# Kernel tuning notes

Measured on AMD Instinct MI355X. Metric: run time of the kernel, lower is better.

Reference implementation:

```python
import jax, jax.numpy as jnp
import numpy as np

IN_CH, C_M, C_N = 512, 512, 128
B, H, W = 16, 56, 56


def setup_inputs() -> dict:
    key = jax.random.key(0)
    ks = jax.random.split(key, 7)
    s = 1.0 / np.sqrt(IN_CH)
    return {
        "x": jax.random.normal(ks[0], (B, IN_CH, H, W), dtype=jnp.float32),
        "wA": jax.random.uniform(ks[1], (C_M, IN_CH), jnp.float32, -s, s),
        "bA": jax.random.uniform(ks[2], (C_M,), jnp.float32, -s, s),
        "wB": jax.random.uniform(ks[3], (C_N, IN_CH), jnp.float32, -s, s),
        "bB": jax.random.uniform(ks[4], (C_N,), jnp.float32, -s, s),
        "wV": jax.random.uniform(ks[5], (C_N, IN_CH), jnp.float32, -s, s),
        "bV": jax.random.uniform(ks[6], (C_N,), jnp.float32, -s, s),
        "K": 1,
    }


def reference(x, wA, bA, wB, bB, wV, bV, K):
    b, c, h, w = x.shape
    c_m, c_n = wA.shape[0], wB.shape[0]
    batch = b // K
    hw = h * w
    N = K * hw
    # 1x1 convs == channel-wise matmuls
    A = jnp.einsum('bchw,mc->bmhw', x, wA) + bA[None, :, None, None]
    Bf = jnp.einsum('bchw,nc->bnhw', x, wB) + bB[None, :, None, None]
    Vf = jnp.einsum('bchw,nc->bnhw', x, wV) + bV[None, :, None, None]
    # (batch, c_m, K*h*w)
    tmpA = A.reshape(batch, K, c_m, hw).transpose(0, 2, 1, 3).reshape(batch, c_m, N)
    # softmax over the spatial dim N (torch Softmax() on 2D -> dim=1)
    tmpB = Bf.reshape(batch, K, c_n, hw).transpose(0, 2, 1, 3).reshape(batch, c_n, N)
    attB = jax.nn.softmax(tmpB, axis=-1).transpose(0, 2, 1)  # (batch, N, c_n)
    # softmax over channel dim c_n
    tmpV = Vf.reshape(batch, K, c_n, hw).transpose(0, 1, 3, 2).reshape(batch, N, c_n)
    attV = jax.nn.softmax(tmpV, axis=-1).transpose(0, 2, 1)  # (batch, c_n, N)
    G = jnp.matmul(tmpA, attB)   # (batch, c_m, c_n) global descriptors
    Z = jnp.matmul(G, attV)      # (batch, c_m, N) distribute
    Z = Z.reshape(batch, c_m, K, hw).transpose(0, 2, 1, 3).reshape(b, c_m, h, w)
    return Z
```

## Files before the change

kernel.cpp:

```cpp
#include <hip/hip_runtime.h>
#include <hip/hip_bf16.h>

#define BATCH 16
#define CIN   512
#define HW    3136
#define CM    512
#define CN    128

typedef short short8 __attribute__((ext_vector_type(8)));
typedef float f32x4  __attribute__((ext_vector_type(4)));

#define MFMA(a,b,c) __builtin_amdgcn_mfma_f32_16x16x32_bf16((a),(b),(c),0,0,0)

__device__ __forceinline__ void cvt_store8(__bf16* dst, const float* src) {
  const f32x4 a = *(const f32x4*)src;
  const f32x4 b = *(const f32x4*)(src + 4);
  __attribute__((aligned(16))) __bf16 t[8];
  t[0] = (__bf16)a[0]; t[1] = (__bf16)a[1]; t[2] = (__bf16)a[2]; t[3] = (__bf16)a[3];
  t[4] = (__bf16)b[0]; t[5] = (__bf16)b[1]; t[6] = (__bf16)b[2]; t[7] = (__bf16)b[3];
  *(uint4*)dst = *(uint4*)t;
}

__device__ __forceinline__ void cvt_store8v(__bf16* dst, f32x4 a, f32x4 b) {
  __attribute__((aligned(16))) __bf16 t[8];
  t[0] = (__bf16)a[0]; t[1] = (__bf16)a[1]; t[2] = (__bf16)a[2]; t[3] = (__bf16)a[3];
  t[4] = (__bf16)b[0]; t[5] = (__bf16)b[1]; t[6] = (__bf16)b[2]; t[7] = (__bf16)b[3];
  *(uint4*)dst = *(uint4*)t;
}

__global__ __launch_bounds__(256) void prep_w_kernel(
    const float* __restrict__ wB, const float* __restrict__ wV,
    __bf16* __restrict__ Wimg)
{
  const int gid  = blockIdx.x * 256 + threadIdx.x;
  const int lane = gid & 63;
  const int kk   = (gid >> 6) & 1;
  const int mi   = (gid >> 7) & 3;
  const int w    = (gid >> 9) & 3;
  const int st   = (gid >> 11) & 7;
  const int row  = w*64 + mi*16 + (lane & 15);
  const int col  = st*64 + kk*32 + (lane >> 4)*8;
  const float* src = (row < 128) ? (wB + (size_t)row * CIN)
                                 : (wV + (size_t)(row - 128) * CIN);
  cvt_store8(Wimg + (size_t)gid * 8, src + col);
}

__global__ __launch_bounds__(256) void conv_bv_kernel(
    const float* __restrict__ x,
    const __bf16* __restrict__ Wimg,
    const float* __restrict__ bB, const float* __restrict__ bV,
    __bf16* __restrict__ BVB, __bf16* __restrict__ attVT,
    float* __restrict__ bsum)
{
  const int s0  = blockIdx.x * 64;
  const int b   = blockIdx.y;
  const int tid = threadIdx.x;
  const int lane = tid & 63, w = tid >> 6;
  const int l15  = lane & 15, q = lane >> 4;

  __shared__ __attribute__((aligned(16))) __bf16 Xt[2][64*72];
  __bf16* T = (__bf16*)Xt;
  __shared__ float Vm[2][64];
  __shared__ float Vs[2][64];

  f32x4 acc[4][4] = {};
  const float* xb = x + (size_t)b*CIN*HW + s0;
  const int colg = tid & 7;
  const int cl = 2*(tid >> 3);
  const int xoff = ((cl >> 3) ^ colg)*8 + (cl & 7);

  const char* wbase = (const char*)Wimg + (size_t)w*8192 + (size_t)lane*16;

  short8 wf[8];
#define WLOAD(ST) do { const char* wp_ = wbase + (ST)*32768; \
    wf[0]=*(const short8*)(wp_+0);    wf[1]=*(const short8*)(wp_+1024); \
    wf[2]=*(const short8*)(wp_+2048); wf[3]=*(const short8*)(wp_+3072); \
    wf[4]=*(const short8*)(wp_+4096); wf[5]=*(const short8*)(wp_+5120); \
    wf[6]=*(const short8*)(wp_+6144); wf[7]=*(const short8*)(wp_+7168); } while(0)

  f32x4 pf[2][4];
#define XLOAD(PB, K0) do { \
    const float* r0_ = xb + (size_t)((K0) + cl)*HW + colg*8; \
    const float* r1_ = r0_ + HW; \
    pf[PB][0] = *(const f32x4*)r0_; pf[PB][1] = *(const f32x4*)(r0_ + 4); \
    pf[PB][2] = *(const f32x4*)r1_; pf[PB][3] = *(const f32x4*)(r1_ + 4); } while(0)

#define XWRITE(BUF, PB) do { \
    _Pragma("unroll") \
    for (int j = 0; j < 8; ++j) { \
      int s_ = colg*8 + j; \
      union { __bf16 h[2]; unsigned int u; } pv_; \
      pv_.h[0] = (__bf16)pf[PB][j>>2][j&3]; \
      pv_.h[1] = (__bf16)pf[PB][2 + (j>>2)][j&3]; \
      *(unsigned int*)&Xt[BUF][s_*72 + xoff] = pv_.u; \
    } } while(0)

  XLOAD(0, 0);
  WLOAD(0);
  XLOAD(1, 64);
  XWRITE(0, 0);
  __syncthreads();

  #pragma unroll
  for (int st = 0; st < 8; ++st) {
    const int cur = st & 1;
    short8 xf0[4];
    #pragma unroll
    for (int si = 0; si < 4; ++si) {
      int s = si*16 + l15;
      int oct = q ^ (si*2 + (l15 >> 3));
      xf0[si] = *(short8*)&Xt[cur][s*72 + oct*8];
    }
    #pragma unroll
    for (int mi = 0; mi < 4; ++mi)
      #pragma unroll
      for (int si = 0; si < 4; ++si)
        acc[mi][si] = MFMA(wf[mi*2], xf0[si], acc[mi][si]);

    if (st < 7) XWRITE(cur ^ 1, (st + 1) & 1);
    if (st < 6) XLOAD(st & 1, (st + 2) * 64);

    short8 xf1[4];
    #pragma unroll
    for (int si = 0; si < 4; ++si) {
      int s = si*16 + l15;
      int oct = (4 + q) ^ (si*2 + (l15 >> 3));
      xf1[si] = *(short8*)&Xt[cur][s*72 + oct*8];
    }
    #pragma unroll
    for (int mi = 0; mi < 4; ++mi)
      #pragma unroll
      for (int si = 0; si < 4; ++si)
        acc[mi][si] = MFMA(wf[mi*2+1], xf1[si], acc[mi][si]);

    if (st < 7) WLOAD(st + 1);
    __syncthreads();
  }
#undef WLOAD
#undef XLOAD
#undef XWRITE

  float bias[4][4];
  #pragma unroll
  for (int mi = 0; mi < 4; ++mi)
    #pragma unroll
    for (int r = 0; r < 4; ++r) {
      int nch = w*64 + mi*16 + q*4 + r;
      bias[mi][r] = (nch < CN) ? bB[nch] : bV[nch - CN];
    }

  if (w < 2) {
    const size_t outb = (size_t)b * CN * HW;
    float psum[4][4] = {};
    #pragma unroll
    for (int mi = 0; mi < 4; ++mi)
      #pragma unroll
      for (int si = 0; si < 4; ++si) {
        int s = s0 + si*16 + l15;
        #pragma unroll
        for (int r = 0; r < 4; ++r) {
          int nch = w*64 + mi*16 + q*4 + r;
          __bf16 bv = (__bf16)(acc[mi][si][r] + bias[mi][r]);
          BVB[outb + (size_t)nch*HW + s] = bv;
          psum[mi][r] += __expf((float)bv);
        }
      }
    #pragma unroll
    for (int mi = 0; mi < 4; ++mi)
      #pragma unroll
      for (int r = 0; r < 4; ++r) {
        float v = psum[mi][r];
        v += __shfl_xor(v, 1); v += __shfl_xor(v, 2);
        v += __shfl_xor(v, 4); v += __shfl_xor(v, 8);
        if (l15 == 0) {
          int nch = w*64 + mi*16 + q*4 + r;
          atomicAdd(&bsum[b*CN + nch], v);
        }
      }
  } else {
    #pragma unroll
    for (int si = 0; si < 4; ++si) {
      float m = -1e30f;
      #pragma unroll
      for (int mi = 0; mi < 4; ++mi)
        #pragma unroll
        for (int r = 0; r < 4; ++r)
          m = fmaxf(m, acc[mi][si][r] + bias[mi][r]);
      m = fmaxf(m, __shfl_xor(m, 16));
      m = fmaxf(m, __shfl_xor(m, 32));
      if (q == 0) Vm[w-2][si*16 + l15] = m;
    }
  }
  __syncthreads();
  if (w >= 2) {
    #pragma unroll
    for (int si = 0; si < 4; ++si) {
      int idx = si*16 + l15;
      float ms = fmaxf(Vm[0][idx], Vm[1][idx]);
      float ssum = 0.f;
      #pragma unroll
      for (int mi = 0; mi < 4; ++mi)
        #pragma unroll
        for (int r = 0; r < 4; ++r) {
          float e = __expf(acc[mi][si][r] + bias[mi][r] - ms);
          acc[mi][si][r] = e;
          ssum += e;
        }
      ssum += __shfl_xor(ssum, 16);
      ssum += __shfl_xor(ssum, 32);
      if (q == 0) Vs[w-2][idx] = ssum;
    }
  }
  __syncthreads();
  if (w >= 2) {
    #pragma unroll
    for (int si = 0; si < 4; ++si) {
      int idx = si*16 + l15;
      float inv = 1.0f / (Vs[0][idx] + Vs[1][idx]);
      #pragma unroll
      for (int mi = 0; mi < 4; ++mi)
        #pragma unroll
        for (int r = 0; r < 4; ++r) {
          int j = (w-2)*64 + mi*16 + q*4 + r;
          T[idx*136 + j] = (__bf16)(acc[mi][si][r] * inv);
        }
    }
  }
  __syncthreads();
  __bf16* dst = attVT + ((size_t)b*HW + s0)*CN;
  #pragma unroll
  for (int k = 0; k < 4; ++k) {
    int chunk = tid + 256*k;
    int row = chunk >> 4, oct = chunk & 15;
    *(uint4*)&dst[(size_t)row*CN + oct*8] = *(uint4*)&T[row*136 + oct*8];
  }
}

__global__ __launch_bounds__(256) void h_gemm_kernel(
    const float* __restrict__ x, const __bf16* __restrict__ BVB,
    const float* __restrict__ bsum, float* __restrict__ H)
{
  const int c0 = blockIdx.x * 64, b = blockIdx.y, kc = blockIdx.z;
  const int tid = threadIdx.x, lane = tid & 63, w = tid >> 6;
  const int l15 = lane & 15, q = lane >> 4;

  __shared__ __attribute__((aligned(16))) __bf16 At[64*72];
  __shared__ __attribute__((aligned(16))) __bf16 Bt[128*72];
  f32x4 acc[4][2] = {};

  const float* xb = x + ((size_t)b*CIN + c0)*HW;
  const __bf16* ab = BVB + (size_t)b*CN*HW;
  const float* bsb = bsum + b*CN;
  const int colg = tid & 7, row0 = tid >> 3;

  float irow[4];
  #pragma unroll
  for (int p = 0; p < 4; ++p) irow[p] = 1.0f / bsb[row0 + 32*p];

  f32x4 px[2][2];
  uint4 pB[4];
#define HLOAD(K0) do { \
    _Pragma("unroll") \
    for (int p = 0; p < 2; ++p) { \
      const float* s_ = xb + (size_t)(row0 + 32*p)*HW + (K0) + colg*8; \
      px[p][0] = *(const f32x4*)s_; px[p][1] = *(const f32x4*)(s_ + 4); \
    } \
    _Pragma("unroll") \
    for (int p = 0; p < 4; ++p) \
      pB[p] = *(const uint4*)(ab + (size_t)(row0 + 32*p)*HW + (K0) + colg*8); \
  } while(0)

  const int kbase = kc * 448;
  HLOAD(kbase);

  for (int ki = 0; ki < 7; ++ki) {
    #pragma unroll
    for (int p = 0; p < 2; ++p)
      cvt_store8v(&At[(row0 + 32*p)*72 + colg*8], px[p][0], px[p][1]);
    #pragma unroll
    for (int p = 0; p < 4; ++p) {
      const __bf16* v = (const __bf16*)&pB[p];
      __attribute__((aligned(16))) __bf16 t[8];
      #pragma unroll
      for (int j = 0; j < 8; ++j)
        t[j] = (__bf16)(__expf((float)v[j]) * irow[p]);
      *(uint4*)&Bt[(row0 + 32*p)*72 + colg*8] = *(uint4*)t;
    }
    if (ki < 6) HLOAD(kbase + (ki + 1)*64);
    __syncthreads();
    #pragma unroll
    for (int kk = 0; kk < 2; ++kk) {
      short8 a[4], bb[2];
      #pragma unroll
      for (int mi = 0; mi < 4; ++mi)
        a[mi] = *(short8*)&At[(mi*16 + l15)*72 + kk*32 + q*8];
      #pragma unroll
      for (int ni = 0; ni < 2; ++ni)
        bb[ni] = *(short8*)&Bt[(w*32 + ni*16 + l15)*72 + kk*32 + q*8];
      #pragma unroll
      for (int mi = 0; mi < 4; ++mi)
        #pragma unroll
        for (int ni = 0; ni < 2; ++ni)
          acc[mi][ni] = MFMA(a[mi], bb[ni], acc[mi][ni]);
    }
    __syncthreads();
  }
#undef HLOAD

  float* Hb = H + (size_t)b*CIN*CN;
  #pragma unroll
  for (int mi = 0; mi < 4; ++mi)
    #pragma unroll
    for (int ni = 0; ni < 2; ++ni)
      #pragma unroll
      for (int r = 0; r < 4; ++r) {
        int c = c0 + mi*16 + q*4 + r;
        int n = w*32 + ni*16 + l15;
        atomicAdd(&Hb[c*CN + n], acc[mi][ni][r]);
      }
}

__global__ __launch_bounds__(256) void g_gemm_kernel(
    const float* __restrict__ wA, const float* __restrict__ bA,
    const float* __restrict__ H, __bf16* __restrict__ G)
{
  const int m0 = blockIdx.x * 64, b = blockIdx.y;
  const int tid = threadIdx.x, lane = tid & 63, w = tid >> 6;
  const int l15 = lane & 15, q = lane >> 4;

  __shared__ __attribute__((aligned(16))) __bf16 At[64*72];
  __shared__ __attribute__((aligned(16))) __bf16 Bt[128*72];
  f32x4 acc[4][2] = {};

  const float* Hb = H + (size_t)b*CIN*CN;
  const int colg = tid & 7, row0 = tid >> 3;
  const int nn = tid & 127, gh = tid >> 7;

  for (int k0 = 0; k0 < CIN; k0 += 64) {
    #pragma unroll
    for (int p = 0; p < 2; ++p) {
      int row = row0 + 32*p;
      cvt_store8(&At[row*72 + colg*8], wA + (size_t)(m0+row)*CIN + k0 + colg*8);
    }
    #pragma unroll
    for (int p = 0; p < 4; ++p) {
      int g = gh + 2*p;
      __attribute__((aligned(16))) __bf16 tmp[8];
      #pragma unroll
      for (int j = 0; j < 8; ++j)
        tmp[j] = (__bf16)Hb[(size_t)(k0 + g*8 + j)*CN + nn];
      *(uint4*)&Bt[nn*72 + g*8] = *(uint4*)tmp;
    }
    __syncthreads();
    #pragma unroll
    for (int kk = 0; kk < 2; ++kk) {
      short8 a[4], bb[2];
      #pragma unroll
      for (int mi = 0; mi < 4; ++mi)
        a[mi] = *(short8*)&At[(mi*16 + l15)*72 + kk*32 + q*8];
      #pragma unroll
      for (int ni = 0; ni < 2; ++ni)
        bb[ni] = *(short8*)&Bt[(w*32 + ni*16 + l15)*72 + kk*32 + q*8];
      #pragma unroll
      for (int mi = 0; mi < 4; ++mi)
        #pragma unroll
        for (int ni = 0; ni < 2; ++ni)
          acc[mi][ni] = MFMA(a[mi], bb[ni], acc[mi][ni]);
    }
    __syncthreads();
  }

  #pragma unroll
  for (int mi = 0; mi < 4; ++mi)
    #pragma unroll
    for (int ni = 0; ni < 2; ++ni)
      #pragma unroll
      for (int r = 0; r < 4; ++r) {
        int m = m0 + mi*16 + q*4 + r;
        int n = w*32 + ni*16 + l15;
        G[((size_t)b*CM + m)*CN + n] = (__bf16)(acc[mi][ni][r] + bA[m]);
      }
}

__global__ __launch_bounds__(256) void z_gemm_kernel(
    const __bf16* __restrict__ G, const __bf16* __restrict__ attVT,
    float* __restrict__ out)
{
  const int m0 = blockIdx.x * 128, s0 = blockIdx.y * 64, b = blockIdx.z;
  const int tid = threadIdx.x, lane = tid & 63, w = tid >> 6;
  const int l15 = lane & 15, q = lane >> 4;

  const __bf16* Gb = G + ((size_t)b*CM + m0)*CN;
  const __bf16* Vb = attVT + ((size_t)b*HW + s0)*CN;

  short8 bb[4];
  const __bf16* vrow = Vb + (size_t)(w*16 + l15)*CN + q*8;
  #pragma unroll
  for (int kk = 0; kk < 4; ++kk)
    bb[kk] = *(const short8*)(vrow + kk*32);

  f32x4 acc[8] = {};
  #pragma unroll
  for (int kk = 0; kk < 4; ++kk) {
    short8 a[8];
    #pragma unroll
    for (int mi = 0; mi < 8; ++mi)
      a[mi] = *(const short8*)(Gb + (size_t)(mi*16 + l15)*CN + kk*32 + q*8);
    #pragma unroll
    for (int mi = 0; mi < 8; ++mi)
      acc[mi] = MFMA(a[mi], bb[kk], acc[mi]);
  }

  const int s = s0 + w*16 + l15;
  #pragma unroll
  for (int mi = 0; mi < 8; ++mi)
    #pragma unroll
    for (int r = 0; r < 4; ++r) {
      int m = m0 + mi*16 + q*4 + r;
      out[((size_t)b*CM + m)*HW + s] = acc[mi][r];
    }
}

extern "C" void kernel_launch(void* const* d_in, const int* in_sizes, int n_in,
                              void* d_out, int out_size, void* d_ws, size_t ws_size,
                              hipStream_t stream)
{
  (void)in_sizes; (void)n_in; (void)out_size; (void)ws_size;
  const float* x  = (const float*)d_in[0];
  const float* wA = (const float*)d_in[1];
  const float* bA = (const float*)d_in[2];
  const float* wB = (const float*)d_in[3];
  const float* bB = (const float*)d_in[4];
  const float* wV = (const float*)d_in[5];
  const float* bV = (const float*)d_in[6];
  float* out = (float*)d_out;

  char* ws = (char*)d_ws;
  const size_t szBVB   = (size_t)BATCH*CN*HW*2;
  const size_t szAttVT = (size_t)BATCH*HW*CN*2;
  const size_t szH     = (size_t)BATCH*CIN*CN*4;
  const size_t szBsum  = (size_t)BATCH*CN*4;
  const size_t szG     = (size_t)BATCH*CM*CN*2;

  char* p = ws;
  __bf16* BVB   = (__bf16*)p; p += szBVB;
  __bf16* attVT = (__bf16*)p; p += szAttVT;
  float*  H     = (float*)p;  p += szH;
  float*  bsum  = (float*)p;  p += szBsum;
  __bf16* G     = (__bf16*)p; p += szG;
  __bf16* Wimg  = (__bf16*)p;

  hipMemsetAsync(H, 0, szH + szBsum, stream);
  prep_w_kernel <<<dim3(64),      256, 0, stream>>>(wB, wV, Wimg);
  conv_bv_kernel<<<dim3(49,16),   256, 0, stream>>>(x, Wimg, bB, bV, BVB, attVT, bsum);
  h_gemm_kernel <<<dim3(8,16,7),  256, 0, stream>>>(x, BVB, bsum, H);
  g_gemm_kernel <<<dim3(8,16),    256, 0, stream>>>(wA, bA, H, G);
  z_gemm_kernel <<<dim3(4,49,16), 256, 0, stream>>>(G, attVT, out);
}
```

Before: 323.3 us.

## Double-buffer weights, lighten barriers, widen H tile, stage Z operands in LDS

In conv_bv, weight fragments are now double-buffered and prefetched at the top of each stage, so global weight loads overlap the MFMAs. __syncthreads is replaced everywhere by a barrier that only waits on LDS counters, leaving global loads in flight across it. h_gemm doubles its channel tile to 128 with half the blocks, so each BVB tile loaded is reused by twice as many channels. z_gemm stages G and attV tiles cooperatively into padded LDS instead of doing strided per-lane global loads. This raises register and LDS use and lowers occupancy and block count in h_gemm.

```diff
diff --git a/kernel.cpp b/kernel.cpp
--- a/kernel.cpp
+++ b/kernel.cpp
@@ -11,6 +11,12 @@
 typedef float f32x4  __attribute__((ext_vector_type(4)));
 
 #define MFMA(a,b,c) __builtin_amdgcn_mfma_f32_16x16x32_bf16((a),(b),(c),0,0,0)
+
+__device__ __forceinline__ void wg_barrier() {
+  asm volatile("s_waitcnt lgkmcnt(0)" ::: "memory");
+  __builtin_amdgcn_s_barrier();
+  asm volatile("" ::: "memory");
+}
 
 __device__ __forceinline__ void cvt_store8(__bf16* dst, const float* src) {
   const f32x4 a = *(const f32x4*)src;
@@ -71,14 +77,15 @@
 
   const char* wbase = (const char*)Wimg + (size_t)w*8192 + (size_t)lane*16;
 
-  short8 wf[8];
-#define WLOAD(ST) do { const char* wp_ = wbase + (ST)*32768; \
-    wf[0]=*(const short8*)(wp_+0);    wf[1]=*(const short8*)(wp_+1024); \
-    wf[2]=*(const short8*)(wp_+2048); wf[3]=*(const short8*)(wp_+3072); \
-    wf[4]=*(const short8*)(wp_+4096); wf[5]=*(const short8*)(wp_+5120); \
-    wf[6]=*(const short8*)(wp_+6144); wf[7]=*(const short8*)(wp_+7168); } while(0)
-
+  short8 wf[2][8];
   f32x4 pf[2][4];
+
+#define WLOAD(WB, ST) do { const char* wp_ = wbase + (ST)*32768; \
+    wf[WB][0]=*(const short8*)(wp_+0);    wf[WB][1]=*(const short8*)(wp_+1024); \
+    wf[WB][2]=*(const short8*)(wp_+2048); wf[WB][3]=*(const short8*)(wp_+3072); \
+    wf[WB][4]=*(const short8*)(wp_+4096); wf[WB][5]=*(const short8*)(wp_+5120); \
+    wf[WB][6]=*(const short8*)(wp_+6144); wf[WB][7]=*(const short8*)(wp_+7168); } while(0)
+
 #define XLOAD(PB, K0) do { \
     const float* r0_ = xb + (size_t)((K0) + cl)*HW + colg*8; \
     const float* r1_ = r0_ + HW; \
@@ -96,14 +103,16 @@
     } } while(0)
 
   XLOAD(0, 0);
-  WLOAD(0);
+  WLOAD(0, 0);
   XLOAD(1, 64);
   XWRITE(0, 0);
-  __syncthreads();
+  wg_barrier();
 
   #pragma unroll
   for (int st = 0; st < 8; ++st) {
     const int cur = st & 1;
+    if (st < 7) WLOAD(cur ^ 1, st + 1);
+
     short8 xf0[4];
     #pragma unroll
     for (int si = 0; si < 4; ++si) {
@@ -115,7 +124,7 @@
     for (int mi = 0; mi < 4; ++mi)
       #pragma unroll
       for (int si = 0; si < 4; ++si)
-        acc[mi][si] = MFMA(wf[mi*2], xf0[si], acc[mi][si]);
+        acc[mi][si] = MFMA(wf[cur][mi*2], xf0[si], acc[mi][si]);
 
     if (st < 7) XWRITE(cur ^ 1, (st + 1) & 1);
     if (st < 6) XLOAD(st & 1, (st + 2) * 64);
@@ -131,10 +140,9 @@
     for (int mi = 0; mi < 4; ++mi)
       #pragma unroll
       for (int si = 0; si < 4; ++si)
-        acc[mi][si] = MFMA(wf[mi*2+1], xf1[si], acc[mi][si]);
-
-    if (st < 7) WLOAD(st + 1);
-    __syncthreads();
+        acc[mi][si] = MFMA(wf[cur][mi*2+1], xf1[si], acc[mi][si]);
+
+    wg_barrier();
   }
 #undef WLOAD
 #undef XLOAD
@@ -191,7 +199,7 @@
       if (q == 0) Vm[w-2][si*16 + l15] = m;
     }
   }
-  __syncthreads();
+  wg_barrier();
   if (w >= 2) {
     #pragma unroll
     for (int si = 0; si < 4; ++si) {
@@ -211,7 +219,7 @@
       if (q == 0) Vs[w-2][idx] = ssum;
     }
   }
-  __syncthreads();
+  wg_barrier();
   if (w >= 2) {
     #pragma unroll
     for (int si = 0; si < 4; ++si) {
@@ -226,7 +234,7 @@
         }
     }
   }
-  __syncthreads();
+  wg_barrier();
   __bf16* dst = attVT + ((size_t)b*HW + s0)*CN;
   #pragma unroll
   for (int k = 0; k < 4; ++k) {
@@ -240,13 +248,13 @@
     const float* __restrict__ x, const __bf16* __restrict__ BVB,
     const float* __restrict__ bsum, float* __restrict__ H)
 {
-  const int c0 = blockIdx.x * 64, b = blockIdx.y, kc = blockIdx.z;
+  const int c0 = blockIdx.x * 128, b = blockIdx.y, kc = blockIdx.z;
   const int tid = threadIdx.x, lane = tid & 63, w = tid >> 6;
   const int l15 = lane & 15, q = lane >> 4;
 
-  __shared__ __attribute__((aligned(16))) __bf16 At[64*72];
+  __shared__ __attribute__((aligned(16))) __bf16 At[128*72];
   __shared__ __attribute__((aligned(16))) __bf16 Bt[128*72];
-  f32x4 acc[4][2] = {};
+  f32x4 acc[8][2] = {};
 
   const float* xb = x + ((size_t)b*CIN + c0)*HW;
   const __bf16* ab = BVB + (size_t)b*CN*HW;
@@ -257,11 +265,11 @@
   #pragma unroll
   for (int p = 0; p < 4; ++p) irow[p] = 1.0f / bsb[row0 + 32*p];
 
-  f32x4 px[2][2];
+  f32x4 px[4][2];
   uint4 pB[4];
 #define HLOAD(K0) do { \
     _Pragma("unroll") \
-    for (int p = 0; p < 2; ++p) { \
+    for (int p = 0; p < 4; ++p) { \
       const float* s_ = xb + (size_t)(row0 + 32*p)*HW + (K0) + colg*8; \
       px[p][0] = *(const f32x4*)s_; px[p][1] = *(const f32x4*)(s_ + 4); \
     } \
@@ -275,7 +283,7 @@
 
   for (int ki = 0; ki < 7; ++ki) {
     #pragma unroll
-    for (int p = 0; p < 2; ++p)
+    for (int p = 0; p < 4; ++p)
       cvt_store8v(&At[(row0 + 32*p)*72 + colg*8], px[p][0], px[p][1]);
     #pragma unroll
     for (int p = 0; p < 4; ++p) {
@@ -287,29 +295,29 @@
       *(uint4*)&Bt[(row0 + 32*p)*72 + colg*8] = *(uint4*)t;
     }
     if (ki < 6) HLOAD(kbase + (ki + 1)*64);
-    __syncthreads();
+    wg_barrier();
     #pragma unroll
     for (int kk = 0; kk < 2; ++kk) {
-      short8 a[4], bb[2];
-      #pragma unroll
-      for (int mi = 0; mi < 4; ++mi)
+      short8 a[8], bb[2];
+      #pragma unroll
+      for (int mi = 0; mi < 8; ++mi)
         a[mi] = *(short8*)&At[(mi*16 + l15)*72 + kk*32 + q*8];
       #pragma unroll
       for (int ni = 0; ni < 2; ++ni)
         bb[ni] = *(short8*)&Bt[(w*32 + ni*16 + l15)*72 + kk*32 + q*8];
       #pragma unroll
-      for (int mi = 0; mi < 4; ++mi)
+      for (int mi = 0; mi < 8; ++mi)
         #pragma unroll
         for (int ni = 0; ni < 2; ++ni)
           acc[mi][ni] = MFMA(a[mi], bb[ni], acc[mi][ni]);
     }
-    __syncthreads();
+    wg_barrier();
   }
 #undef HLOAD
 
   float* Hb = H + (size_t)b*CIN*CN;
   #pragma unroll
-  for (int mi = 0; mi < 4; ++mi)
+  for (int mi = 0; mi < 8; ++mi)
     #pragma unroll
     for (int ni = 0; ni < 2; ++ni)
       #pragma unroll
@@ -351,7 +359,7 @@
         tmp[j] = (__bf16)Hb[(size_t)(k0 + g*8 + j)*CN + nn];
       *(uint4*)&Bt[nn*72 + g*8] = *(uint4*)tmp;
     }
-    __syncthreads();
+    wg_barrier();
     #pragma unroll
     for (int kk = 0; kk < 2; ++kk) {
       short8 a[4], bb[2];
@@ -367,7 +375,7 @@
         for (int ni = 0; ni < 2; ++ni)
           acc[mi][ni] = MFMA(a[mi], bb[ni], acc[mi][ni]);
     }
-    __syncthreads();
+    wg_barrier();
   }
 
   #pragma unroll
@@ -390,25 +398,33 @@
   const int tid = threadIdx.x, lane = tid & 63, w = tid >> 6;
   const int l15 = lane & 15, q = lane >> 4;
 
+  __shared__ __attribute__((aligned(16))) __bf16 At[128*136];
+  __shared__ __attribute__((aligned(16))) __bf16 Bt[64*136];
+
   const __bf16* Gb = G + ((size_t)b*CM + m0)*CN;
   const __bf16* Vb = attVT + ((size_t)b*HW + s0)*CN;
-
-  short8 bb[4];
-  const __bf16* vrow = Vb + (size_t)(w*16 + l15)*CN + q*8;
-  #pragma unroll
-  for (int kk = 0; kk < 4; ++kk)
-    bb[kk] = *(const short8*)(vrow + kk*32);
+  const int g = tid & 15, r0 = tid >> 4;
+  #pragma unroll
+  for (int p = 0; p < 8; ++p) {
+    int row = r0 + 16*p;
+    *(uint4*)&At[row*136 + g*8] = *(const uint4*)(Gb + (size_t)row*CN + g*8);
+  }
+  #pragma unroll
+  for (int p = 0; p < 4; ++p) {
+    int row = r0 + 16*p;
+    *(uint4*)&Bt[row*136 + g*8] = *(const uint4*)(Vb + (size_t)row*CN + g*8);
+  }
+  wg_barrier();
 
   f32x4 acc[8] = {};
   #pragma unroll
   for (int kk = 0; kk < 4; ++kk) {
-    short8 a[8];
-    #pragma unroll
-    for (int mi = 0; mi < 8; ++mi)
-      a[mi] = *(const short8*)(Gb + (size_t)(mi*16 + l15)*CN + kk*32 + q*8);
-    #pragma unroll
-    for (int mi = 0; mi < 8; ++mi)
-      acc[mi] = MFMA(a[mi], bb[kk], acc[mi]);
+    short8 bb = *(short8*)&Bt[(w*16 + l15)*136 + kk*32 + q*8];
+    #pragma unroll
+    for (int mi = 0; mi < 8; ++mi) {
+      short8 a = *(short8*)&At[(mi*16 + l15)*136 + kk*32 + q*8];
+      acc[mi] = MFMA(a, bb, acc[mi]);
+    }
   }
 
   const int s = s0 + w*16 + l15;
@@ -453,7 +469,7 @@
   hipMemsetAsync(H, 0, szH + szBsum, stream);
   prep_w_kernel <<<dim3(64),      256, 0, stream>>>(wB, wV, Wimg);
   conv_bv_kernel<<<dim3(49,16),   256, 0, stream>>>(x, Wimg, bB, bV, BVB, attVT, bsum);
-  h_gemm_kernel <<<dim3(8,16,7),  256, 0, stream>>>(x, BVB, bsum, H);
+  h_gemm_kernel <<<dim3(4,16,7),  256, 0, stream>>>(x, BVB, bsum, H);
   g_gemm_kernel <<<dim3(8,16),    256, 0, stream>>>(wA, bA, H, G);
   z_gemm_kernel <<<dim3(4,49,16), 256, 0, stream>>>(G, attVT, out);
 }
```

Result: faster. 283.9 us (-12.2%).
